# Kernel tuning notes

Hardware: AMD Instinct MI355X
Metric: run time of the kernel (lower is better)

Reference implementation:

```python
import jax, jax.numpy as jnp
import numpy as np

EPS = 1e-08
F_DIM = 512


def setup_inputs() -> dict:
    key = jax.random.key(0)
    ks = jax.random.split(key, 7)
    N, F = 50000, F_DIM
    q = jax.random.normal(ks[0], (N, 1, F), dtype=jnp.float32)
    mu = jax.random.normal(ks[1], (N, 3, F), dtype=jnp.float32)
    # Xavier-ish scaled params
    W_mix = jax.random.normal(ks[2], (2 * F, F), dtype=jnp.float32) * (1.0 / np.sqrt(F))
    W1 = jax.random.normal(ks[3], (F, 2 * F), dtype=jnp.float32) * (1.0 / np.sqrt(2 * F))
    b1 = jnp.zeros((F,), dtype=jnp.float32)
    W2 = jax.random.normal(ks[4], (3 * F, F), dtype=jnp.float32) * (1.0 / np.sqrt(F))
    b2 = jnp.zeros((3 * F,), dtype=jnp.float32)
    return {"q": q, "mu": mu, "W_mix": W_mix, "W1": W1, "b1": b1, "W2": W2, "b2": b2}


def reference(q, mu, W_mix, W1, b1, W2, b2):
    F = q.shape[-1]
    # mu_channel_mix: [N,3,F] @ [F,2F] -> [N,3,2F]
    mu_mix = jnp.einsum('ndf,gf->ndg', mu, W_mix)
    mu_V, mu_W = mu_mix[..., :F], mu_mix[..., F:]
    # vector norm over Cartesian axis -> [N,1,F]
    mu_Vn = jnp.sqrt(jnp.sum(mu_V * mu_V, axis=-2, keepdims=True) + EPS)
    ctx = jnp.concatenate([q, mu_Vn], axis=-1)  # [N,1,2F]
    h = jax.nn.silu(jnp.einsum('nsf,gf->nsg', ctx, W1) + b1)  # [N,1,F]
    x = jnp.einsum('nsf,gf->nsg', h, W2) + b2  # [N,1,3F]
    dq_intra = x[..., :F]
    dmu_intra = x[..., F:2 * F] * mu_W  # broadcast [N,1,F]*[N,3,F]
    dqmu_intra = x[..., 2 * F:] * jnp.sum(mu_V * mu_W, axis=1, keepdims=True)
    q_out = q + dq_intra + dqmu_intra
    mu_out = mu + dmu_intra
    return (q_out, mu_out)
```

## Files before the change

### kernel.cpp

```cpp
#include <hip/hip_runtime.h>
#include <stdint.h>

#define NN 50000
#define QWORDS 25600000

typedef __attribute__((ext_vector_type(8))) short bf16x8;
typedef __attribute__((ext_vector_type(4))) float f32x4;

__device__ __forceinline__ uint32_t f2bf(float x){
  uint32_t u = __builtin_bit_cast(uint32_t, x);
  u += 0x7FFFu + ((u >> 16) & 1u);
  return u >> 16;
}
__device__ __forceinline__ float bf2f(uint32_t b){
  uint32_t u = b << 16;
  return __builtin_bit_cast(float, u);
}
__device__ __forceinline__ void gload16(const uint16_t* g, uint16_t* l){
  __builtin_amdgcn_global_load_lds(
      (const __attribute__((address_space(1))) uint32_t*)g,
      (__attribute__((address_space(3))) uint32_t*)l, 16, 0, 0);
}
__device__ __forceinline__ f32x4 mfma16(bf16x8 a, bf16x8 b, f32x4 c){
  return __builtin_amdgcn_mfma_f32_16x16x32_bf16(a, b, c, 0, 0, 0);
}

#define FENCE() asm volatile("" ::: "memory")

__global__ void k_convert(const float* __restrict__ wmix, const float* __restrict__ w1,
                          const float* __restrict__ w2, uint16_t* __restrict__ dst){
  int i = blockIdx.x * 256 + threadIdx.x;
  int e = i << 2;
  const float* s; int o;
  if (e < 524288)       { s = wmix; o = e; }
  else if (e < 1048576) { s = w1;   o = e - 524288; }
  else                  { s = w2;   o = e - 1048576; }
  f32x4 v = *(const f32x4*)(s + o);
  uint2 pk;
  pk.x = f2bf(v[0]) | (f2bf(v[1]) << 16);
  pk.y = f2bf(v[2]) | (f2bf(v[3]) << 16);
  *(uint2*)(dst + e) = pk;
}

__global__ __launch_bounds__(512, 4)
void k_gemm1(const float* __restrict__ mu, const uint16_t* __restrict__ wmixb,
             uint16_t* __restrict__ qh, float* __restrict__ muW){
  __shared__ uint16_t As[2][12288];
  __shared__ uint16_t Bs[2][8192];
  const int tid  = threadIdx.x;
  const int lane = tid & 63;
  const int w    = tid >> 6;
  const int wn   = w & 3;
  const int wf   = w >> 2;
  const int orig = blockIdx.x;
  const int j    = (orig & 7) * 782 + (orig >> 3);
  const int f0   = (j & 7) * 64;
  const int n0   = (j >> 3) * 64;
  const int lrow = tid >> 4;
  const int lcol = (tid & 15) * 4;

  f32x4 ar[6];
  auto A_LOAD = [&](int ks){
    const int k0 = ks * 64;
    #pragma unroll
    for (int p=0; p<6; ++p){
      int r = p*32 + lrow;
      int d = r >> 6, nrow = r & 63;
      int n = n0 + nrow;
      int g = (n < NN ? n : NN-1)*3 + d;
      ar[p] = *(const f32x4*)(mu + (size_t)g*512 + k0 + lcol);
    }
  };
  auto A_WRITE = [&](int buf){
    #pragma unroll
    for (int p=0; p<6; ++p){
      int r = p*32 + lrow;
      f32x4 v = ar[p];
      uint2 pk;
      pk.x = f2bf(v[0]) | (f2bf(v[1]) << 16);
      pk.y = f2bf(v[2]) | (f2bf(v[3]) << 16);
      *(uint2*)&As[buf][r*64 + (lcol ^ ((r&7)<<3))] = pk;
    }
  };
  auto B_ISSUE = [&](int ks, int buf){
    const int k0 = ks * 64;
    #pragma unroll
    for (int jj=0; jj<2; ++jj){
      int jb = w*2 + jj;
      int row = jb*8 + (lane>>3);
      int g = (row < 64) ? (f0 + row) : (448 + f0 + row);
      int srcc = ((lane&7) ^ ((lane>>3)&7)) * 8;
      gload16(wmixb + (size_t)g*512 + k0 + srcc, &Bs[buf][jb*512]);
    }
  };

  const f32x4 z4 = {0.f,0.f,0.f,0.f};
  f32x4 acc[3][4];
  #pragma unroll
  for (int d=0; d<3; ++d)
    #pragma unroll
    for (int nt=0; nt<4; ++nt) acc[d][nt] = z4;

  A_LOAD(0); B_ISSUE(0, 0); A_WRITE(0);
  for (int ks=0; ks<8; ++ks){
    const int cur = ks & 1;
    __syncthreads();
    if (ks < 7){ A_LOAD(ks+1); B_ISSUE(ks+1, cur^1); }
    #pragma unroll
    for (int kf=0; kf<2; ++kf){
      int kc = kf*32 + (lane>>4)*8;
      bf16x8 af[3];
      #pragma unroll
      for (int d=0; d<3; ++d){
        int r = d*64 + wn*16 + (lane&15);
        af[d] = *(const bf16x8*)&As[cur][r*64 + (kc ^ ((r&7)<<3))];
      }
      #pragma unroll
      for (int nt=0; nt<4; ++nt){
        int ntg = wf*2 + (nt&1) + (nt>>1)*4;
        int rr = ntg*16 + (lane&15);
        bf16x8 bf = *(const bf16x8*)&Bs[cur][rr*64 + (kc ^ ((rr&7)<<3))];
        #pragma unroll
        for (int d=0; d<3; ++d)
          acc[d][nt] = mfma16(bf, af[d], acc[d][nt]);
      }
    }
    if (ks < 7) A_WRITE(cur^1);
  }

  const int rb4 = (lane >> 4) * 4;
  const int nthr = n0 + wn*16 + (lane & 15);
  if (nthr < NN){
    #pragma unroll
    for (int c=0; c<2; ++c){
      int f = f0 + (wf*2 + c)*16 + rb4;
      uint2 pkv, pkd; f32x4 u0v, u1v, u2v;
      uint32_t vb[4], db[4];
      #pragma unroll
      for (int p=0; p<4; ++p){
        float v0 = acc[0][c][p],   v1 = acc[1][c][p],   v2 = acc[2][c][p];
        float u0 = acc[0][c+2][p], u1 = acc[1][c+2][p], u2 = acc[2][c+2][p];
        float vn = sqrtf(v0*v0 + v1*v1 + v2*v2 + 1e-8f);
        float dt = v0*u0 + v1*u1 + v2*u2;
        vb[p] = f2bf(vn); db[p] = f2bf(dt);
        u0v[p] = u0; u1v[p] = u1; u2v[p] = u2;
      }
      pkv.x = vb[0] | (vb[1] << 16); pkv.y = vb[2] | (vb[3] << 16);
      pkd.x = db[0] | (db[1] << 16); pkd.y = db[2] | (db[3] << 16);
      *(uint2*)(qh + (size_t)nthr*1024 + f)       = pkv;
      *(uint2*)(qh + (size_t)nthr*1024 + 512 + f) = pkd;
      size_t mb = (size_t)nthr*1536 + f;
      *(f32x4*)(muW + mb)        = u0v;
      *(f32x4*)(muW + mb + 512)  = u1v;
      *(f32x4*)(muW + mb + 1024) = u2v;
    }
  }
}

__global__ __launch_bounds__(512, 4)
void k_gemm1b(const float* __restrict__ mu, const uint16_t* __restrict__ wmixb,
              uint16_t* __restrict__ qh, uint16_t* __restrict__ mw16){
  __shared__ uint16_t As[2][12288];
  __shared__ uint16_t Bs[2][8192];
  const int tid  = threadIdx.x;
  const int lane = tid & 63;
  const int w    = tid >> 6;
  const int wn   = w & 3;
  const int wf   = w >> 2;
  const int orig = blockIdx.x;
  const int j    = (orig & 7) * 782 + (orig >> 3);
  const int f0   = (j & 7) * 64;
  const int n0   = (j >> 3) * 64;
  const int lrow = tid >> 4;
  const int lcol = (tid & 15) * 4;

  f32x4 ar[6];
  auto A_LOAD = [&](int ks){
    const int k0 = ks * 64;
    #pragma unroll
    for (int p=0; p<6; ++p){
      int r = p*32 + lrow;
      int d = r >> 6, nrow = r & 63;
      int n = n0 + nrow;
      int g = (n < NN ? n : NN-1)*3 + d;
      ar[p] = *(const f32x4*)(mu + (size_t)g*512 + k0 + lcol);
    }
  };
  auto A_WRITE = [&](int buf){
    #pragma unroll
    for (int p=0; p<6; ++p){
      int r = p*32 + lrow;
      f32x4 v = ar[p];
      uint2 pk;
      pk.x = f2bf(v[0]) | (f2bf(v[1]) << 16);
      pk.y = f2bf(v[2]) | (f2bf(v[3]) << 16);
      *(uint2*)&As[buf][r*64 + (lcol ^ ((r&7)<<3))] = pk;
    }
  };
  auto B_ISSUE = [&](int ks, int buf){
    const int k0 = ks * 64;
    #pragma unroll
    for (int jj=0; jj<2; ++jj){
      int jb = w*2 + jj;
      int row = jb*8 + (lane>>3);
      int g = (row < 64) ? (f0 + row) : (448 + f0 + row);
      int srcc = ((lane&7) ^ ((lane>>3)&7)) * 8;
      gload16(wmixb + (size_t)g*512 + k0 + srcc, &Bs[buf][jb*512]);
    }
  };

  const f32x4 z4 = {0.f,0.f,0.f,0.f};
  f32x4 acc[3][4];
  #pragma unroll
  for (int d=0; d<3; ++d)
    #pragma unroll
    for (int nt=0; nt<4; ++nt) acc[d][nt] = z4;

  A_LOAD(0); B_ISSUE(0, 0); A_WRITE(0);
  for (int ks=0; ks<8; ++ks){
    const int cur = ks & 1;
    __syncthreads();
    if (ks < 7){ A_LOAD(ks+1); B_ISSUE(ks+1, cur^1); }
    #pragma unroll
    for (int kf=0; kf<2; ++kf){
      int kc = kf*32 + (lane>>4)*8;
      bf16x8 af[3];
      #pragma unroll
      for (int d=0; d<3; ++d){
        int r = d*64 + wn*16 + (lane&15);
        af[d] = *(const bf16x8*)&As[cur][r*64 + (kc ^ ((r&7)<<3))];
      }
      #pragma unroll
      for (int nt=0; nt<4; ++nt){
        int ntg = wf*2 + (nt&1) + (nt>>1)*4;
        int rr = ntg*16 + (lane&15);
        bf16x8 bf = *(const bf16x8*)&Bs[cur][rr*64 + (kc ^ ((rr&7)<<3))];
        #pragma unroll
        for (int d=0; d<3; ++d)
          acc[d][nt] = mfma16(bf, af[d], acc[d][nt]);
      }
    }
    if (ks < 7) A_WRITE(cur^1);
  }

  const int rb4 = (lane >> 4) * 4;
  const int nthr = n0 + wn*16 + (lane & 15);
  if (nthr < NN){
    #pragma unroll
    for (int c=0; c<2; ++c){
      int f = f0 + (wf*2 + c)*16 + rb4;
      uint2 pkv, pkd, pw0, pw1, pw2;
      uint32_t vb[4], db[4], w0[4], w1[4], w2[4];
      #pragma unroll
      for (int p=0; p<4; ++p){
        float v0 = acc[0][c][p],   v1 = acc[1][c][p],   v2 = acc[2][c][p];
        float u0 = acc[0][c+2][p], u1 = acc[1][c+2][p], u2 = acc[2][c+2][p];
        float vn = sqrtf(v0*v0 + v1*v1 + v2*v2 + 1e-8f);
        float dt = v0*u0 + v1*u1 + v2*u2;
        vb[p] = f2bf(vn); db[p] = f2bf(dt);
        w0[p] = f2bf(u0); w1[p] = f2bf(u1); w2[p] = f2bf(u2);
      }
      pkv.x = vb[0] | (vb[1] << 16); pkv.y = vb[2] | (vb[3] << 16);
      pkd.x = db[0] | (db[1] << 16); pkd.y = db[2] | (db[3] << 16);
      pw0.x = w0[0] | (w0[1] << 16); pw0.y = w0[2] | (w0[3] << 16);
      pw1.x = w1[0] | (w1[1] << 16); pw1.y = w1[2] | (w1[3] << 16);
      pw2.x = w2[0] | (w2[1] << 16); pw2.y = w2[2] | (w2[3] << 16);
      *(uint2*)(qh + (size_t)nthr*1024 + f)       = pkv;
      *(uint2*)(qh + (size_t)nthr*1024 + 512 + f) = pkd;
      size_t mb = (size_t)nthr*1536 + f;
      *(uint2*)(mw16 + mb)        = pw0;
      *(uint2*)(mw16 + mb + 512)  = pw1;
      *(uint2*)(mw16 + mb + 1024) = pw2;
    }
  }
}

__global__ __launch_bounds__(512, 4)
void k_gemm2(const float* __restrict__ q, const uint16_t* __restrict__ w1b,
             const float* __restrict__ b1, uint16_t* __restrict__ qh){
  __shared__ uint16_t A2[2][2048];
  __shared__ uint16_t B2[2][16384];
  const int tid  = threadIdx.x;
  const int lane = tid & 63;
  const int w    = tid >> 6;
  const int wm   = w >> 2;
  const int wn   = w & 3;
  const int n0   = blockIdx.x * 64;

  f32x4 qa;
  auto QA_LOAD = [&](int s){
    int k0 = s*32;
    int row = tid >> 3, ch = tid & 7;
    int nc = (n0 + row < NN) ? n0 + row : NN-1;
    qa = *(const f32x4*)(q + (size_t)nc*512 + k0 + ch*4);
  };
  auto QA_WRITE = [&](int buf){
    int row = tid >> 3, ch = tid & 7;
    uint2 pk;
    pk.x = f2bf(qa[0]) | (f2bf(qa[1]) << 16);
    pk.y = f2bf(qa[2]) | (f2bf(qa[3]) << 16);
    *(uint2*)&A2[buf][row*32 + (((ch>>1) ^ (row&3))<<3) + (ch&1)*4] = pk;
  };
  auto VA_ISSUE = [&](int s, int buf){
    if (w < 4){
      int k0v = (s-16)*32;
      int row = w*16 + (lane>>2);
      int nc = (n0 + row < NN) ? n0 + row : NN-1;
      int srcch = (lane&3) ^ (row&3);
      gload16(qh + (size_t)nc*1024 + k0v + srcch*8, &A2[buf][w*512]);
    }
  };
  auto B_ISSUE = [&](int s, int buf){
    int k0 = s*32;
    #pragma unroll
    for (int jj=0; jj<4; ++jj){
      int j = w*4 + jj;
      int row = j*16 + (lane>>2);
      int srcch = (lane&3) ^ (row&3);
      gload16(w1b + (size_t)row*1024 + k0 + srcch*8, &B2[buf][j*512]);
    }
  };

  const f32x4 z4 = {0.f,0.f,0.f,0.f};
  f32x4 acc2[2][8];
  #pragma unroll
  for (int mt=0; mt<2; ++mt)
    #pragma unroll
    for (int nt=0; nt<8; ++nt) acc2[mt][nt] = z4;

  QA_LOAD(0); B_ISSUE(0, 0); QA_WRITE(0);
  for (int s=0; s<32; ++s){
    const int cur = s & 1;
    __syncthreads();
    if (s < 31){
      if (s+1 < 16) QA_LOAD(s+1); else VA_ISSUE(s+1, cur^1);
      B_ISSUE(s+1, cur^1);
    }
    {
      int kc = (lane>>4)*8;
      bf16x8 a[2];
      #pragma unroll
      for (int mt=0; mt<2; ++mt){
        int r = wm*32 + mt*16 + (lane&15);
        a[mt] = *(const bf16x8*)&A2[cur][r*32 + (kc ^ ((r&3)<<3))];
      }
      #pragma unroll
      for (int nt=0; nt<8; ++nt){
        int rr = wn*128 + nt*16 + (lane&15);
        bf16x8 b = *(const bf16x8*)&B2[cur][rr*32 + (kc ^ ((rr&3)<<3))];
        acc2[0][nt] = mfma16(a[0], b, acc2[0][nt]);
        acc2[1][nt] = mfma16(a[1], b, acc2[1][nt]);
      }
    }
    if (s < 31 && s+1 < 16) QA_WRITE(cur^1);
  }

  const int rb4 = (lane >> 4) * 4;
  #pragma unroll
  for (int nt=0; nt<8; ++nt){
    int col = wn*128 + nt*16 + (lane&15);
    float bb = b1[col];
    #pragma unroll
    for (int mt=0; mt<2; ++mt)
      #pragma unroll
      for (int j=0; j<4; ++j){
        int n = n0 + wm*32 + mt*16 + rb4 + j;
        if (n < NN){
          float x = acc2[mt][nt][j] + bb;
          float sv = x / (1.f + __expf(-x));
          qh[(size_t)n*1024 + col] = (uint16_t)f2bf(sv);
        }
      }
  }
}

__global__ __launch_bounds__(256, 4)
void k_gemm3c(const float* __restrict__ q, const float* __restrict__ mu,
              const uint16_t* __restrict__ w2b, const float* __restrict__ b2,
              float* __restrict__ dout, const uint16_t* __restrict__ mw16){
  __shared__ uint16_t Hs[16*512];
  __shared__ uint16_t B3[2][6144];
  const int tid  = threadIdx.x;
  const int lane = tid & 63;
  const int w    = tid >> 6;
  const int n0   = blockIdx.x * 16;
  const uint16_t* qh = (const uint16_t*)dout;
  float* mout = dout + (size_t)QWORDS;
  const int l15 = lane & 15;
  const int rb4 = (lane >> 4) * 4;
  const f32x4 z4 = {0.f,0.f,0.f,0.f};

  #pragma unroll
  for (int i=0; i<4; ++i){
    int row = w*4 + i;
    int nc2 = (n0 + row < NN) ? n0 + row : NN-1;
    gload16(qh + (size_t)nc2*1024 + (size_t)((lane ^ (row&7))*8), &Hs[row*512]);
  }

  auto B_ISSUE = [&](int it, int ks, uint16_t* slot){
    #pragma unroll
    for (int jj=0; jj<3; ++jj){
      int j = w*3 + jj;
      int rr = j*16 + (lane>>2);
      int s3 = rr >> 6, fi = rr & 63;
      int g = s3*512 + it*64 + fi;
      int srcc = ((lane&3) ^ (rr&3)) * 8;
      gload16(w2b + (size_t)g*512 + ks*32 + srcc, slot + j*512);
    }
  };
  B_ISSUE(0, 0, B3[0]);

  const int nthr = n0 + l15;
  const int nc   = nthr < NN ? nthr : NN-1;

  f32x4 qv, bbv[3], muv[3], mwv[3];
  float dtv[4];
  int   fb = 0;
  f32x4 acc3[3];

#define K3C_MFMA(P) do{ \
    const uint16_t* bsl = B3[(P)&1]; \
    __builtin_amdgcn_s_setprio(1); \
    { \
      int r = l15; \
      int ch = ((P)*4 + (lane>>4)) ^ (r&7); \
      bf16x8 a = *(const bf16x8*)&Hs[r*512 + ch*8]; \
      _Pragma("unroll") \
      for (int s3=0; s3<3; ++s3){ \
        int rr = s3*64 + w*16 + l15; \
        int chb = (lane>>4) ^ (rr&3); \
        bf16x8 b = *(const bf16x8*)&bsl[rr*32 + chb*8]; \
        acc3[s3] = mfma16(b, a, acc3[s3]); \
      } \
    } \
    __builtin_amdgcn_s_setprio(0); \
  } while(0)

#define K3C_PHASE(P, WAIT) \
    asm volatile("s_waitcnt vmcnt(" #WAIT ")" ::: "memory"); \
    __builtin_amdgcn_s_barrier(); \
    B_ISSUE(it, (P)+1, B3[((P)+1)&1]); \
    FENCE(); \
    K3C_MFMA(P);

  #pragma unroll 1
  for (int it=0; it<8; ++it){
    if (it) { asm volatile("s_waitcnt vmcnt(4)" ::: "memory"); }
    else    { asm volatile("s_waitcnt vmcnt(0)" ::: "memory"); }
    __builtin_amdgcn_s_barrier();
    B_ISSUE(it, 1, B3[1]);
    FENCE();
    {
      #pragma unroll
      for (int s3=0; s3<3; ++s3) acc3[s3] = z4;
      fb = it*64 + w*16 + rb4;
      bbv[0] = *(const f32x4*)(b2 + fb);
      bbv[1] = *(const f32x4*)(b2 + 512 + fb);
      bbv[2] = *(const f32x4*)(b2 + 1024 + fb);
      uint2 du = *(const uint2*)(qh + (size_t)nc*1024 + 512 + fb);
      dtv[0] = bf2f(du.x & 0xffff); dtv[1] = bf2f(du.x >> 16);
      dtv[2] = bf2f(du.y & 0xffff); dtv[3] = bf2f(du.y >> 16);
      qv = *(const f32x4*)(q + (size_t)nc*512 + fb);
    }
    FENCE();
    K3C_MFMA(0);

    asm volatile("s_waitcnt vmcnt(5)" ::: "memory");
    __builtin_amdgcn_s_barrier();
    B_ISSUE(it, 2, B3[0]);
    FENCE();
    {
      size_t mb = (size_t)nc*1536 + fb;
      muv[0] = *(const f32x4*)(mu + mb);
      muv[1] = *(const f32x4*)(mu + mb + 512);
      muv[2] = *(const f32x4*)(mu + mb + 1024);
    }
    FENCE();
    K3C_MFMA(1);

    asm volatile("s_waitcnt vmcnt(3)" ::: "memory");
    __builtin_amdgcn_s_barrier();
    B_ISSUE(it, 3, B3[1]);
    FENCE();
    {
      size_t mb = (size_t)nc*1536 + fb;
      uint2 a0 = *(const uint2*)(mw16 + mb);
      uint2 a1 = *(const uint2*)(mw16 + mb + 512);
      uint2 a2 = *(const uint2*)(mw16 + mb + 1024);
      mwv[0][0]=bf2f(a0.x&0xffff); mwv[0][1]=bf2f(a0.x>>16);
      mwv[0][2]=bf2f(a0.y&0xffff); mwv[0][3]=bf2f(a0.y>>16);
      mwv[1][0]=bf2f(a1.x&0xffff); mwv[1][1]=bf2f(a1.x>>16);
      mwv[1][2]=bf2f(a1.y&0xffff); mwv[1][3]=bf2f(a1.y>>16);
      mwv[2][0]=bf2f(a2.x&0xffff); mwv[2][1]=bf2f(a2.x>>16);
      mwv[2][2]=bf2f(a2.y&0xffff); mwv[2][3]=bf2f(a2.y>>16);
    }
    FENCE();
    K3C_MFMA(2);

    K3C_PHASE(3, 3)
    K3C_PHASE(4, 0)
    K3C_PHASE(5, 0)
    K3C_PHASE(6, 0)
    K3C_PHASE(7, 0)
    K3C_PHASE(8, 0)
    K3C_PHASE(9, 0)
    K3C_PHASE(10, 0)
    K3C_PHASE(11, 0)
    K3C_PHASE(12, 0)
    K3C_PHASE(13, 0)
    K3C_PHASE(14, 0)

    asm volatile("s_waitcnt vmcnt(0)" ::: "memory");
    __builtin_amdgcn_s_barrier();
    if (it < 7) B_ISSUE(it+1, 0, B3[0]);
    FENCE();
    K3C_MFMA(15);
    if (nthr < NN){
      f32x4 qo, m0, m1, m2;
      #pragma unroll
      for (int p=0; p<4; ++p){
        float x0 = acc3[0][p] + bbv[0][p];
        float x1 = acc3[1][p] + bbv[1][p];
        float x2 = acc3[2][p] + bbv[2][p];
        qo[p] = qv[p] + x0 + x2*dtv[p];
        m0[p] = muv[0][p] + x1*mwv[0][p];
        m1[p] = muv[1][p] + x1*mwv[1][p];
        m2[p] = muv[2][p] + x1*mwv[2][p];
      }
      *(f32x4*)(dout + (size_t)nthr*512 + fb) = qo;
      size_t mb = (size_t)nthr*1536 + fb;
      *(f32x4*)(mout + mb)        = m0;
      *(f32x4*)(mout + mb + 512)  = m1;
      *(f32x4*)(mout + mb + 1024) = m2;
    }
  }
#undef K3C_PHASE
#undef K3C_MFMA
}

__global__ __launch_bounds__(512, 4)
void k_gemm3(const float* __restrict__ q, const float* __restrict__ mu,
             const uint16_t* __restrict__ w2b, const float* __restrict__ b2,
             float* __restrict__ dout){
  __shared__ uint16_t Hs[32*512];
  __shared__ uint16_t B3[2][12288];
  const int tid  = threadIdx.x;
  const int lane = tid & 63;
  const int w    = tid >> 6;
  const int wm   = w >> 2;
  const int wn   = w & 3;
  const int n0   = blockIdx.x * 32;
  const uint16_t* qh = (const uint16_t*)dout;
  float* mout = dout + (size_t)QWORDS;
  const int l15 = lane & 15;
  const int rb4 = (lane >> 4) * 4;
  const f32x4 z4 = {0.f,0.f,0.f,0.f};

  #pragma unroll
  for (int i=0; i<4; ++i){
    int row = w*4 + i;
    int nc2 = (n0 + row < NN) ? n0 + row : NN-1;
    gload16(qh + (size_t)nc2*1024 + (size_t)((lane ^ (row&7))*8), &Hs[row*512]);
  }

  auto B_ISSUE = [&](int it, int ks, uint16_t* slot){
    #pragma unroll
    for (int jj=0; jj<3; ++jj){
      int jx = w*3 + jj;
      int rr = jx*8 + (lane>>3);
      int s3 = rr >> 6, fi = rr & 63;
      int g = s3*512 + it*64 + fi;
      gload16(w2b + (size_t)g*512 + ks*64 + ((lane&7) ^ (rr&7))*8, slot + jx*512);
    }
  };
  B_ISSUE(0, 0, B3[0]);

  const int nthr = n0 + wm*16 + l15;
  const int nc   = nthr < NN ? nthr : NN-1;

  f32x4 qv, bbv[3], muv[3], mwv[3];
  float dtv[4];
  int   fb = 0;
  f32x4 acc3[3];

#define K3_MFMA(KS) do{ \
    const uint16_t* bsl = B3[(KS)&1]; \
    __builtin_amdgcn_s_setprio(1); \
    _Pragma("unroll") \
    for (int kf=0; kf<2; ++kf){ \
      int r = wm*16 + l15; \
      int ch = ((KS)*8 + kf*4 + (lane>>4)) ^ (r&7); \
      bf16x8 a = *(const bf16x8*)&Hs[r*512 + ch*8]; \
      _Pragma("unroll") \
      for (int s3=0; s3<3; ++s3){ \
        int rr = s3*64 + wn*16 + l15; \
        int chb = (kf*4 + (lane>>4)) ^ (rr&7); \
        bf16x8 b = *(const bf16x8*)&bsl[rr*64 + chb*8]; \
        acc3[s3] = mfma16(b, a, acc3[s3]); \
      } \
    } \
    __builtin_amdgcn_s_setprio(0); \
  } while(0)

  #pragma unroll 1
  for (int it=0; it<8; ++it){
    if (it) { asm volatile("s_waitcnt vmcnt(4)" ::: "memory"); }
    else    { asm volatile("s_waitcnt vmcnt(0)" ::: "memory"); }
    __builtin_amdgcn_s_barrier();
    B_ISSUE(it, 1, B3[1]);
    FENCE();
    {
      #pragma unroll
      for (int s3=0; s3<3; ++s3) acc3[s3] = z4;
      fb = it*64 + wn*16 + rb4;
      bbv[0] = *(const f32x4*)(b2 + fb);
      bbv[1] = *(const f32x4*)(b2 + 512 + fb);
      bbv[2] = *(const f32x4*)(b2 + 1024 + fb);
      uint2 du = *(const uint2*)(qh + (size_t)nc*1024 + 512 + fb);
      dtv[0] = bf2f(du.x & 0xffff); dtv[1] = bf2f(du.x >> 16);
      dtv[2] = bf2f(du.y & 0xffff); dtv[3] = bf2f(du.y >> 16);
      qv = *(const f32x4*)(q + (size_t)nc*512 + fb);
    }
    FENCE();
    K3_MFMA(0);

    asm volatile("s_waitcnt vmcnt(5)" ::: "memory");
    __builtin_amdgcn_s_barrier();
    B_ISSUE(it, 2, B3[0]);
    FENCE();
    {
      size_t mb = (size_t)nc*1536 + fb;
      muv[0] = *(const f32x4*)(mu + mb);
      muv[1] = *(const f32x4*)(mu + mb + 512);
      muv[2] = *(const f32x4*)(mu + mb + 1024);
    }
    FENCE();
    K3_MFMA(1);

    asm volatile("s_waitcnt vmcnt(3)" ::: "memory");
    __builtin_amdgcn_s_barrier();
    B_ISSUE(it, 3, B3[1]);
    FENCE();
    {
      size_t mb = (size_t)nc*1536 + fb;
      mwv[0] = *(const f32x4*)(mout + mb);
      mwv[1] = *(const f32x4*)(mout + mb + 512);
      mwv[2] = *(const f32x4*)(mout + mb + 1024);
    }
    FENCE();
    K3_MFMA(2);

    asm volatile("s_waitcnt vmcnt(3)" ::: "memory");
    __builtin_amdgcn_s_barrier();
    B_ISSUE(it, 4, B3[0]);
    FENCE();
    K3_MFMA(3);

    asm volatile("s_waitcnt vmcnt(0)" ::: "memory");
    __builtin_amdgcn_s_barrier();
    B_ISSUE(it, 5, B3[1]);
    FENCE();
    K3_MFMA(4);

    asm volatile("s_waitcnt vmcnt(0)" ::: "memory");
    __builtin_amdgcn_s_barrier();
    B_ISSUE(it, 6, B3[0]);
    FENCE();
    K3_MFMA(5);

    asm volatile("s_waitcnt vmcnt(0)" ::: "memory");
    __builtin_amdgcn_s_barrier();
    B_ISSUE(it, 7, B3[1]);
    FENCE();
    K3_MFMA(6);

    asm volatile("s_waitcnt vmcnt(0)" ::: "memory");
    __builtin_amdgcn_s_barrier();
    if (it < 7) B_ISSUE(it+1, 0, B3[0]);
    FENCE();
    K3_MFMA(7);
    if (nthr < NN){
      f32x4 qo, m0, m1, m2;
      #pragma unroll
      for (int p=0; p<4; ++p){
        float x0 = acc3[0][p] + bbv[0][p];
        float x1 = acc3[1][p] + bbv[1][p];
        float x2 = acc3[2][p] + bbv[2][p];
        qo[p] = qv[p] + x0 + x2*dtv[p];
        m0[p] = muv[0][p] + x1*mwv[0][p];
        m1[p] = muv[1][p] + x1*mwv[1][p];
        m2[p] = muv[2][p] + x1*mwv[2][p];
      }
      *(f32x4*)(dout + (size_t)nthr*512 + fb) = qo;
      size_t mb = (size_t)nthr*1536 + fb;
      *(f32x4*)(mout + mb)        = m0;
      *(f32x4*)(mout + mb + 512)  = m1;
      *(f32x4*)(mout + mb + 1024) = m2;
    }
  }
#undef K3_MFMA
}

extern "C" void kernel_launch(void* const* d_in, const int* in_sizes, int n_in,
                              void* d_out, int out_size, void* d_ws, size_t ws_size,
                              hipStream_t stream){
  (void)in_sizes; (void)n_in; (void)out_size;
  const float* q    = (const float*)d_in[0];
  const float* mu   = (const float*)d_in[1];
  const float* wmix = (const float*)d_in[2];
  const float* w1   = (const float*)d_in[3];
  const float* b1   = (const float*)d_in[4];
  const float* w2   = (const float*)d_in[5];
  const float* b2   = (const float*)d_in[6];
  uint16_t* wb = (uint16_t*)d_ws;
  float* dout = (float*)d_out;

  hipLaunchKernelGGL(k_convert, dim3(1792), dim3(256), 0, stream, wmix, w1, w2, wb);

  const size_t need = ((size_t)1835008 + (size_t)NN*1536) * 2;
  if (ws_size >= need){
    uint16_t* mw16 = wb + 1835008;
    hipLaunchKernelGGL(k_gemm1b, dim3(6256), dim3(512), 0, stream,
                       mu, wb, (uint16_t*)d_out, mw16);
    hipLaunchKernelGGL(k_gemm2, dim3(782), dim3(512), 0, stream,
                       q, wb + 524288, b1, (uint16_t*)d_out);
    hipLaunchKernelGGL(k_gemm3c, dim3(3125), dim3(256), 0, stream,
                       q, mu, wb + 1048576, b2, dout, mw16);
  } else {
    hipLaunchKernelGGL(k_gemm1, dim3(6256), dim3(512), 0, stream,
                       mu, wb, (uint16_t*)d_out, dout + (size_t)QWORDS);
    hipLaunchKernelGGL(k_gemm2, dim3(782), dim3(512), 0, stream,
                       q, wb + 524288, b1, (uint16_t*)d_out);
    hipLaunchKernelGGL(k_gemm3, dim3(1563), dim3(512), 0, stream,
                       q, mu, wb + 1048576, b2, dout);
  }
}
```

Measured before the change: 972.7 us.

## Warp-specialize final GEMM into producer and consumer waves with 32-row tiles

Replaces the 256-thread, 16-row third-GEMM kernel with a 512-thread kernel. Four waves only stream W2 tiles into a double-buffered LDS slot, and four compute waves each handle two 16-row MFMA groups over a wider K step of 64. Doubling the rows per block halves the weight traffic per output row. Moving global-to-LDS issue off the compute waves is meant to keep the MFMA stream uninterrupted. In exchange, half the waves do no math, the grid is halved and the block uses more LDS, which may lower occupancy and the overlap across blocks.

```diff
diff --git a/kernel.cpp b/kernel.cpp
--- a/kernel.cpp
+++ b/kernel.cpp
@@ -374,21 +374,20 @@
   }
 }
 
-__global__ __launch_bounds__(256, 4)
-void k_gemm3c(const float* __restrict__ q, const float* __restrict__ mu,
+__global__ __launch_bounds__(512, 4)
+void k_gemm3d(const float* __restrict__ q, const float* __restrict__ mu,
               const uint16_t* __restrict__ w2b, const float* __restrict__ b2,
               float* __restrict__ dout, const uint16_t* __restrict__ mw16){
-  __shared__ uint16_t Hs[16*512];
-  __shared__ uint16_t B3[2][6144];
+  __shared__ uint16_t Hs[32*512];
+  __shared__ uint16_t B3[2][12288];
   const int tid  = threadIdx.x;
   const int lane = tid & 63;
   const int w    = tid >> 6;
-  const int n0   = blockIdx.x * 16;
+  const int n0   = blockIdx.x * 32;
   const uint16_t* qh = (const uint16_t*)dout;
   float* mout = dout + (size_t)QWORDS;
   const int l15 = lane & 15;
   const int rb4 = (lane >> 4) * 4;
-  const f32x4 z4 = {0.f,0.f,0.f,0.f};
 
   #pragma unroll
   for (int i=0; i<4; ++i){
@@ -397,145 +396,163 @@
     gload16(qh + (size_t)nc2*1024 + (size_t)((lane ^ (row&7))*8), &Hs[row*512]);
   }
 
-  auto B_ISSUE = [&](int it, int ks, uint16_t* slot){
-    #pragma unroll
-    for (int jj=0; jj<3; ++jj){
-      int j = w*3 + jj;
-      int rr = j*16 + (lane>>2);
-      int s3 = rr >> 6, fi = rr & 63;
-      int g = s3*512 + it*64 + fi;
-      int srcc = ((lane&3) ^ (rr&3)) * 8;
-      gload16(w2b + (size_t)g*512 + ks*32 + srcc, slot + j*512);
-    }
-  };
-  B_ISSUE(0, 0, B3[0]);
-
-  const int nthr = n0 + l15;
-  const int nc   = nthr < NN ? nthr : NN-1;
-
-  f32x4 qv, bbv[3], muv[3], mwv[3];
-  float dtv[4];
-  int   fb = 0;
-  f32x4 acc3[3];
-
-#define K3C_MFMA(P) do{ \
-    const uint16_t* bsl = B3[(P)&1]; \
+  if (w >= 4){
+    const int pw = w - 4;
+    auto B_ISSUE = [&](int it, int ks){
+      uint16_t* slot = B3[ks & 1];
+      #pragma unroll
+      for (int jj=0; jj<6; ++jj){
+        int jx = pw*6 + jj;
+        int rr = jx*8 + (lane>>3);
+        int s3 = rr >> 6, fi = rr & 63;
+        int g = s3*512 + it*64 + fi;
+        gload16(w2b + (size_t)g*512 + ks*64 + ((lane&7) ^ (rr&7))*8, slot + jx*512);
+      }
+    };
+    B_ISSUE(0, 0);
+    asm volatile("s_waitcnt vmcnt(0)" ::: "memory");
+    __syncthreads();
+    #pragma unroll 1
+    for (int it=0; it<8; ++it){
+      #pragma unroll
+      for (int p=0; p<8; ++p){
+        int nit = it, nks = p+1;
+        if (nks == 8){ nks = 0; nit = it+1; }
+        if (nit < 8) B_ISSUE(nit, nks);
+        asm volatile("s_waitcnt vmcnt(0)" ::: "memory");
+        __builtin_amdgcn_s_barrier();
+      }
+    }
+  } else {
+    const int cw = w;
+    asm volatile("s_waitcnt vmcnt(0)" ::: "memory");
+    __syncthreads();
+    const int nth0 = n0 + l15, nth1 = n0 + 16 + l15;
+    const int nc0 = nth0 < NN ? nth0 : NN-1;
+    const int nc1 = nth1 < NN ? nth1 : NN-1;
+    const f32x4 z4 = {0.f,0.f,0.f,0.f};
+    f32x4 acc3[2][3];
+    f32x4 qv0, qv1, bbv[3], muv0[3], muv1[3];
+    uint2 du0, du1, mwu0[3], mwu1[3];
+    int fb = 0;
+
+#define K3D_MFMA(KS) do{ \
+    const uint16_t* bsl = B3[(KS)&1]; \
     __builtin_amdgcn_s_setprio(1); \
-    { \
-      int r = l15; \
-      int ch = ((P)*4 + (lane>>4)) ^ (r&7); \
-      bf16x8 a = *(const bf16x8*)&Hs[r*512 + ch*8]; \
+    _Pragma("unroll") \
+    for (int kf=0; kf<2; ++kf){ \
+      int ch = ((KS)*8 + kf*4 + (lane>>4)) ^ (l15&7); \
+      bf16x8 a0 = *(const bf16x8*)&Hs[l15*512 + ch*8]; \
+      bf16x8 a1 = *(const bf16x8*)&Hs[(16+l15)*512 + ch*8]; \
       _Pragma("unroll") \
       for (int s3=0; s3<3; ++s3){ \
-        int rr = s3*64 + w*16 + l15; \
-        int chb = (lane>>4) ^ (rr&3); \
-        bf16x8 b = *(const bf16x8*)&bsl[rr*32 + chb*8]; \
-        acc3[s3] = mfma16(b, a, acc3[s3]); \
+        int rr = s3*64 + cw*16 + l15; \
+        int chb = (kf*4 + (lane>>4)) ^ (rr&7); \
+        bf16x8 b = *(const bf16x8*)&bsl[rr*64 + chb*8]; \
+        acc3[0][s3] = mfma16(b, a0, acc3[0][s3]); \
+        acc3[1][s3] = mfma16(b, a1, acc3[1][s3]); \
       } \
     } \
     __builtin_amdgcn_s_setprio(0); \
   } while(0)
 
-#define K3C_PHASE(P, WAIT) \
-    asm volatile("s_waitcnt vmcnt(" #WAIT ")" ::: "memory"); \
-    __builtin_amdgcn_s_barrier(); \
-    B_ISSUE(it, (P)+1, B3[((P)+1)&1]); \
-    FENCE(); \
-    K3C_MFMA(P);
-
-  #pragma unroll 1
-  for (int it=0; it<8; ++it){
-    if (it) { asm volatile("s_waitcnt vmcnt(4)" ::: "memory"); }
-    else    { asm volatile("s_waitcnt vmcnt(0)" ::: "memory"); }
-    __builtin_amdgcn_s_barrier();
-    B_ISSUE(it, 1, B3[1]);
-    FENCE();
-    {
-      #pragma unroll
-      for (int s3=0; s3<3; ++s3) acc3[s3] = z4;
-      fb = it*64 + w*16 + rb4;
+    #pragma unroll 1
+    for (int it=0; it<8; ++it){
+      #pragma unroll
+      for (int m=0; m<2; ++m)
+        #pragma unroll
+        for (int s3=0; s3<3; ++s3) acc3[m][s3] = z4;
+      fb = it*64 + cw*16 + rb4;
       bbv[0] = *(const f32x4*)(b2 + fb);
       bbv[1] = *(const f32x4*)(b2 + 512 + fb);
       bbv[2] = *(const f32x4*)(b2 + 1024 + fb);
-      uint2 du = *(const uint2*)(qh + (size_t)nc*1024 + 512 + fb);
-      dtv[0] = bf2f(du.x & 0xffff); dtv[1] = bf2f(du.x >> 16);
-      dtv[2] = bf2f(du.y & 0xffff); dtv[3] = bf2f(du.y >> 16);
-      qv = *(const f32x4*)(q + (size_t)nc*512 + fb);
-    }
-    FENCE();
-    K3C_MFMA(0);
-
-    asm volatile("s_waitcnt vmcnt(5)" ::: "memory");
-    __builtin_amdgcn_s_barrier();
-    B_ISSUE(it, 2, B3[0]);
-    FENCE();
-    {
-      size_t mb = (size_t)nc*1536 + fb;
-      muv[0] = *(const f32x4*)(mu + mb);
-      muv[1] = *(const f32x4*)(mu + mb + 512);
-      muv[2] = *(const f32x4*)(mu + mb + 1024);
-    }
-    FENCE();
-    K3C_MFMA(1);
-
-    asm volatile("s_waitcnt vmcnt(3)" ::: "memory");
-    __builtin_amdgcn_s_barrier();
-    B_ISSUE(it, 3, B3[1]);
-    FENCE();
-    {
-      size_t mb = (size_t)nc*1536 + fb;
-      uint2 a0 = *(const uint2*)(mw16 + mb);
-      uint2 a1 = *(const uint2*)(mw16 + mb + 512);
-      uint2 a2 = *(const uint2*)(mw16 + mb + 1024);
-      mwv[0][0]=bf2f(a0.x&0xffff); mwv[0][1]=bf2f(a0.x>>16);
-      mwv[0][2]=bf2f(a0.y&0xffff); mwv[0][3]=bf2f(a0.y>>16);
-      mwv[1][0]=bf2f(a1.x&0xffff); mwv[1][1]=bf2f(a1.x>>16);
-      mwv[1][2]=bf2f(a1.y&0xffff); mwv[1][3]=bf2f(a1.y>>16);
-      mwv[2][0]=bf2f(a2.x&0xffff); mwv[2][1]=bf2f(a2.x>>16);
-      mwv[2][2]=bf2f(a2.y&0xffff); mwv[2][3]=bf2f(a2.y>>16);
-    }
-    FENCE();
-    K3C_MFMA(2);
-
-    K3C_PHASE(3, 3)
-    K3C_PHASE(4, 0)
-    K3C_PHASE(5, 0)
-    K3C_PHASE(6, 0)
-    K3C_PHASE(7, 0)
-    K3C_PHASE(8, 0)
-    K3C_PHASE(9, 0)
-    K3C_PHASE(10, 0)
-    K3C_PHASE(11, 0)
-    K3C_PHASE(12, 0)
-    K3C_PHASE(13, 0)
-    K3C_PHASE(14, 0)
-
-    asm volatile("s_waitcnt vmcnt(0)" ::: "memory");
-    __builtin_amdgcn_s_barrier();
-    if (it < 7) B_ISSUE(it+1, 0, B3[0]);
-    FENCE();
-    K3C_MFMA(15);
-    if (nthr < NN){
-      f32x4 qo, m0, m1, m2;
-      #pragma unroll
-      for (int p=0; p<4; ++p){
-        float x0 = acc3[0][p] + bbv[0][p];
-        float x1 = acc3[1][p] + bbv[1][p];
-        float x2 = acc3[2][p] + bbv[2][p];
-        qo[p] = qv[p] + x0 + x2*dtv[p];
-        m0[p] = muv[0][p] + x1*mwv[0][p];
-        m1[p] = muv[1][p] + x1*mwv[1][p];
-        m2[p] = muv[2][p] + x1*mwv[2][p];
-      }
-      *(f32x4*)(dout + (size_t)nthr*512 + fb) = qo;
-      size_t mb = (size_t)nthr*1536 + fb;
-      *(f32x4*)(mout + mb)        = m0;
-      *(f32x4*)(mout + mb + 512)  = m1;
-      *(f32x4*)(mout + mb + 1024) = m2;
-    }
-  }
-#undef K3C_PHASE
-#undef K3C_MFMA
+      du0 = *(const uint2*)(qh + (size_t)nc0*1024 + 512 + fb);
+      du1 = *(const uint2*)(qh + (size_t)nc1*1024 + 512 + fb);
+      qv0 = *(const f32x4*)(q + (size_t)nc0*512 + fb);
+      qv1 = *(const f32x4*)(q + (size_t)nc1*512 + fb);
+      FENCE();
+      K3D_MFMA(0);
+      __builtin_amdgcn_s_barrier();
+
+      {
+        size_t mb0 = (size_t)nc0*1536 + fb, mb1 = (size_t)nc1*1536 + fb;
+        muv0[0] = *(const f32x4*)(mu + mb0);
+        muv0[1] = *(const f32x4*)(mu + mb0 + 512);
+        muv0[2] = *(const f32x4*)(mu + mb0 + 1024);
+        muv1[0] = *(const f32x4*)(mu + mb1);
+        muv1[1] = *(const f32x4*)(mu + mb1 + 512);
+        muv1[2] = *(const f32x4*)(mu + mb1 + 1024);
+      }
+      FENCE();
+      K3D_MFMA(1);
+      __builtin_amdgcn_s_barrier();
+
+      {
+        size_t mb0 = (size_t)nc0*1536 + fb, mb1 = (size_t)nc1*1536 + fb;
+        mwu0[0] = *(const uint2*)(mw16 + mb0);
+        mwu0[1] = *(const uint2*)(mw16 + mb0 + 512);
+        mwu0[2] = *(const uint2*)(mw16 + mb0 + 1024);
+        mwu1[0] = *(const uint2*)(mw16 + mb1);
+        mwu1[1] = *(const uint2*)(mw16 + mb1 + 512);
+        mwu1[2] = *(const uint2*)(mw16 + mb1 + 1024);
+      }
+      FENCE();
+      K3D_MFMA(2);
+      __builtin_amdgcn_s_barrier();
+
+      K3D_MFMA(3); __builtin_amdgcn_s_barrier();
+      K3D_MFMA(4); __builtin_amdgcn_s_barrier();
+      K3D_MFMA(5); __builtin_amdgcn_s_barrier();
+      K3D_MFMA(6); __builtin_amdgcn_s_barrier();
+
+      K3D_MFMA(7);
+      asm volatile("s_waitcnt vmcnt(0)" ::: "memory");
+      {
+        auto dec = [&](uint2 u, int p)->float{
+          uint32_t h = (p & 2) ? u.y : u.x;
+          return bf2f((p & 1) ? (h >> 16) : (h & 0xffffu));
+        };
+        if (nth0 < NN){
+          f32x4 qo, mo0, mo1, mo2;
+          #pragma unroll
+          for (int p=0; p<4; ++p){
+            float x0 = acc3[0][0][p] + bbv[0][p];
+            float x1 = acc3[0][1][p] + bbv[1][p];
+            float x2 = acc3[0][2][p] + bbv[2][p];
+            qo[p]  = qv0[p] + x0 + x2*dec(du0, p);
+            mo0[p] = muv0[0][p] + x1*dec(mwu0[0], p);
+            mo1[p] = muv0[1][p] + x1*dec(mwu0[1], p);
+            mo2[p] = muv0[2][p] + x1*dec(mwu0[2], p);
+          }
+          *(f32x4*)(dout + (size_t)nth0*512 + fb) = qo;
+          size_t mb = (size_t)nth0*1536 + fb;
+          *(f32x4*)(mout + mb)        = mo0;
+          *(f32x4*)(mout + mb + 512)  = mo1;
+          *(f32x4*)(mout + mb + 1024) = mo2;
+        }
+        if (nth1 < NN){
+          f32x4 qo, mo0, mo1, mo2;
+          #pragma unroll
+          for (int p=0; p<4; ++p){
+            float x0 = acc3[1][0][p] + bbv[0][p];
+            float x1 = acc3[1][1][p] + bbv[1][p];
+            float x2 = acc3[1][2][p] + bbv[2][p];
+            qo[p]  = qv1[p] + x0 + x2*dec(du1, p);
+            mo0[p] = muv1[0][p] + x1*dec(mwu1[0], p);
+            mo1[p] = muv1[1][p] + x1*dec(mwu1[1], p);
+            mo2[p] = muv1[2][p] + x1*dec(mwu1[2], p);
+          }
+          *(f32x4*)(dout + (size_t)nth1*512 + fb) = qo;
+          size_t mb = (size_t)nth1*1536 + fb;
+          *(f32x4*)(mout + mb)        = mo0;
+          *(f32x4*)(mout + mb + 512)  = mo1;
+          *(f32x4*)(mout + mb + 1024) = mo2;
+        }
+      }
+      __builtin_amdgcn_s_barrier();
+    }
+#undef K3D_MFMA
+  }
 }
 
 __global__ __launch_bounds__(512, 4)
@@ -724,7 +741,7 @@
                        mu, wb, (uint16_t*)d_out, mw16);
     hipLaunchKernelGGL(k_gemm2, dim3(782), dim3(512), 0, stream,
                        q, wb + 524288, b1, (uint16_t*)d_out);
-    hipLaunchKernelGGL(k_gemm3c, dim3(3125), dim3(256), 0, stream,
+    hipLaunchKernelGGL(k_gemm3d, dim3(1563), dim3(512), 0, stream,
                        q, mu, wb + 1048576, b2, dout, mw16);
   } else {
     hipLaunchKernelGGL(k_gemm1, dim3(6256), dim3(512), 0, stream,
```

Result: faster. 899.6 us (-7.5%).

## Replace 16-row gemm3c with 32-row 512-thread gemm3b issuing epilogue loads early

Applied to the files above, without the earlier changes.

Swaps the final GEMM kernel from 16-row, 256-thread blocks with 16 k-phases to 32-row, 512-thread blocks with 8 k-phases of k=64. All epilogue operands (q, mu, the bf16 mu_W, the dt term) are loaded at the start of each output tile instead of spread across phases. The bf16 values are kept packed in registers and unpacked only in the epilogue to save registers. The aim is fewer barriers per tile and more reuse of each weight tile across rows, at the cost of larger blocks, more LDS per block, and long-latency loads held in flight.

```diff
diff --git a/kernel.cpp b/kernel.cpp
--- a/kernel.cpp
+++ b/kernel.cpp
@@ -374,174 +374,10 @@
   }
 }
 
-__global__ __launch_bounds__(256, 4)
-void k_gemm3c(const float* __restrict__ q, const float* __restrict__ mu,
+__global__ __launch_bounds__(512, 4)
+void k_gemm3b(const float* __restrict__ q, const float* __restrict__ mu,
               const uint16_t* __restrict__ w2b, const float* __restrict__ b2,
               float* __restrict__ dout, const uint16_t* __restrict__ mw16){
-  __shared__ uint16_t Hs[16*512];
-  __shared__ uint16_t B3[2][6144];
-  const int tid  = threadIdx.x;
-  const int lane = tid & 63;
-  const int w    = tid >> 6;
-  const int n0   = blockIdx.x * 16;
-  const uint16_t* qh = (const uint16_t*)dout;
-  float* mout = dout + (size_t)QWORDS;
-  const int l15 = lane & 15;
-  const int rb4 = (lane >> 4) * 4;
-  const f32x4 z4 = {0.f,0.f,0.f,0.f};
-
-  #pragma unroll
-  for (int i=0; i<4; ++i){
-    int row = w*4 + i;
-    int nc2 = (n0 + row < NN) ? n0 + row : NN-1;
-    gload16(qh + (size_t)nc2*1024 + (size_t)((lane ^ (row&7))*8), &Hs[row*512]);
-  }
-
-  auto B_ISSUE = [&](int it, int ks, uint16_t* slot){
-    #pragma unroll
-    for (int jj=0; jj<3; ++jj){
-      int j = w*3 + jj;
-      int rr = j*16 + (lane>>2);
-      int s3 = rr >> 6, fi = rr & 63;
-      int g = s3*512 + it*64 + fi;
-      int srcc = ((lane&3) ^ (rr&3)) * 8;
-      gload16(w2b + (size_t)g*512 + ks*32 + srcc, slot + j*512);
-    }
-  };
-  B_ISSUE(0, 0, B3[0]);
-
-  const int nthr = n0 + l15;
-  const int nc   = nthr < NN ? nthr : NN-1;
-
-  f32x4 qv, bbv[3], muv[3], mwv[3];
-  float dtv[4];
-  int   fb = 0;
-  f32x4 acc3[3];
-
-#define K3C_MFMA(P) do{ \
-    const uint16_t* bsl = B3[(P)&1]; \
-    __builtin_amdgcn_s_setprio(1); \
-    { \
-      int r = l15; \
-      int ch = ((P)*4 + (lane>>4)) ^ (r&7); \
-      bf16x8 a = *(const bf16x8*)&Hs[r*512 + ch*8]; \
-      _Pragma("unroll") \
-      for (int s3=0; s3<3; ++s3){ \
-        int rr = s3*64 + w*16 + l15; \
-        int chb = (lane>>4) ^ (rr&3); \
-        bf16x8 b = *(const bf16x8*)&bsl[rr*32 + chb*8]; \
-        acc3[s3] = mfma16(b, a, acc3[s3]); \
-      } \
-    } \
-    __builtin_amdgcn_s_setprio(0); \
-  } while(0)
-
-#define K3C_PHASE(P, WAIT) \
-    asm volatile("s_waitcnt vmcnt(" #WAIT ")" ::: "memory"); \
-    __builtin_amdgcn_s_barrier(); \
-    B_ISSUE(it, (P)+1, B3[((P)+1)&1]); \
-    FENCE(); \
-    K3C_MFMA(P);
-
-  #pragma unroll 1
-  for (int it=0; it<8; ++it){
-    if (it) { asm volatile("s_waitcnt vmcnt(4)" ::: "memory"); }
-    else    { asm volatile("s_waitcnt vmcnt(0)" ::: "memory"); }
-    __builtin_amdgcn_s_barrier();
-    B_ISSUE(it, 1, B3[1]);
-    FENCE();
-    {
-      #pragma unroll
-      for (int s3=0; s3<3; ++s3) acc3[s3] = z4;
-      fb = it*64 + w*16 + rb4;
-      bbv[0] = *(const f32x4*)(b2 + fb);
-      bbv[1] = *(const f32x4*)(b2 + 512 + fb);
-      bbv[2] = *(const f32x4*)(b2 + 1024 + fb);
-      uint2 du = *(const uint2*)(qh + (size_t)nc*1024 + 512 + fb);
-      dtv[0] = bf2f(du.x & 0xffff); dtv[1] = bf2f(du.x >> 16);
-      dtv[2] = bf2f(du.y & 0xffff); dtv[3] = bf2f(du.y >> 16);
-      qv = *(const f32x4*)(q + (size_t)nc*512 + fb);
-    }
-    FENCE();
-    K3C_MFMA(0);
-
-    asm volatile("s_waitcnt vmcnt(5)" ::: "memory");
-    __builtin_amdgcn_s_barrier();
-    B_ISSUE(it, 2, B3[0]);
-    FENCE();
-    {
-      size_t mb = (size_t)nc*1536 + fb;
-      muv[0] = *(const f32x4*)(mu + mb);
-      muv[1] = *(const f32x4*)(mu + mb + 512);
-      muv[2] = *(const f32x4*)(mu + mb + 1024);
-    }
-    FENCE();
-    K3C_MFMA(1);
-
-    asm volatile("s_waitcnt vmcnt(3)" ::: "memory");
-    __builtin_amdgcn_s_barrier();
-    B_ISSUE(it, 3, B3[1]);
-    FENCE();
-    {
-      size_t mb = (size_t)nc*1536 + fb;
-      uint2 a0 = *(const uint2*)(mw16 + mb);
-      uint2 a1 = *(const uint2*)(mw16 + mb + 512);
-      uint2 a2 = *(const uint2*)(mw16 + mb + 1024);
-      mwv[0][0]=bf2f(a0.x&0xffff); mwv[0][1]=bf2f(a0.x>>16);
-      mwv[0][2]=bf2f(a0.y&0xffff); mwv[0][3]=bf2f(a0.y>>16);
-      mwv[1][0]=bf2f(a1.x&0xffff); mwv[1][1]=bf2f(a1.x>>16);
-      mwv[1][2]=bf2f(a1.y&0xffff); mwv[1][3]=bf2f(a1.y>>16);
-      mwv[2][0]=bf2f(a2.x&0xffff); mwv[2][1]=bf2f(a2.x>>16);
-      mwv[2][2]=bf2f(a2.y&0xffff); mwv[2][3]=bf2f(a2.y>>16);
-    }
-    FENCE();
-    K3C_MFMA(2);
-
-    K3C_PHASE(3, 3)
-    K3C_PHASE(4, 0)
-    K3C_PHASE(5, 0)
-    K3C_PHASE(6, 0)
-    K3C_PHASE(7, 0)
-    K3C_PHASE(8, 0)
-    K3C_PHASE(9, 0)
-    K3C_PHASE(10, 0)
-    K3C_PHASE(11, 0)
-    K3C_PHASE(12, 0)
-    K3C_PHASE(13, 0)
-    K3C_PHASE(14, 0)
-
-    asm volatile("s_waitcnt vmcnt(0)" ::: "memory");
-    __builtin_amdgcn_s_barrier();
-    if (it < 7) B_ISSUE(it+1, 0, B3[0]);
-    FENCE();
-    K3C_MFMA(15);
-    if (nthr < NN){
-      f32x4 qo, m0, m1, m2;
-      #pragma unroll
-      for (int p=0; p<4; ++p){
-        float x0 = acc3[0][p] + bbv[0][p];
-        float x1 = acc3[1][p] + bbv[1][p];
-        float x2 = acc3[2][p] + bbv[2][p];
-        qo[p] = qv[p] + x0 + x2*dtv[p];
-        m0[p] = muv[0][p] + x1*mwv[0][p];
-        m1[p] = muv[1][p] + x1*mwv[1][p];
-        m2[p] = muv[2][p] + x1*mwv[2][p];
-      }
-      *(f32x4*)(dout + (size_t)nthr*512 + fb) = qo;
-      size_t mb = (size_t)nthr*1536 + fb;
-      *(f32x4*)(mout + mb)        = m0;
-      *(f32x4*)(mout + mb + 512)  = m1;
-      *(f32x4*)(mout + mb + 1024) = m2;
-    }
-  }
-#undef K3C_PHASE
-#undef K3C_MFMA
-}
-
-__global__ __launch_bounds__(512, 4)
-void k_gemm3(const float* __restrict__ q, const float* __restrict__ mu,
-             const uint16_t* __restrict__ w2b, const float* __restrict__ b2,
-             float* __restrict__ dout){
   __shared__ uint16_t Hs[32*512];
   __shared__ uint16_t B3[2][12288];
   const int tid  = threadIdx.x;
@@ -578,10 +414,10 @@
   const int nthr = n0 + wm*16 + l15;
   const int nc   = nthr < NN ? nthr : NN-1;
 
-  f32x4 qv, bbv[3], muv[3], mwv[3];
-  float dtv[4];
-  int   fb = 0;
-  f32x4 acc3[3];
+  f32x4 qv, bbv[3], muv[3];
+  uint2  du, mwu[3];
+  int    fb = 0;
+  f32x4  acc3[3];
 
 #define K3_MFMA(KS) do{ \
     const uint16_t* bsl = B3[(KS)&1]; \
@@ -616,6 +452,168 @@
       bbv[0] = *(const f32x4*)(b2 + fb);
       bbv[1] = *(const f32x4*)(b2 + 512 + fb);
       bbv[2] = *(const f32x4*)(b2 + 1024 + fb);
+      du = *(const uint2*)(qh + (size_t)nc*1024 + 512 + fb);
+      qv = *(const f32x4*)(q + (size_t)nc*512 + fb);
+      size_t mb = (size_t)nc*1536 + fb;
+      muv[0] = *(const f32x4*)(mu + mb);
+      muv[1] = *(const f32x4*)(mu + mb + 512);
+      muv[2] = *(const f32x4*)(mu + mb + 1024);
+      mwu[0] = *(const uint2*)(mw16 + mb);
+      mwu[1] = *(const uint2*)(mw16 + mb + 512);
+      mwu[2] = *(const uint2*)(mw16 + mb + 1024);
+    }
+    FENCE();
+    K3_MFMA(0);
+
+    asm volatile("s_waitcnt vmcnt(11)" ::: "memory");
+    __builtin_amdgcn_s_barrier();
+    B_ISSUE(it, 2, B3[0]);
+    FENCE();
+    K3_MFMA(1);
+
+    asm volatile("s_waitcnt vmcnt(0)" ::: "memory");
+    __builtin_amdgcn_s_barrier();
+    B_ISSUE(it, 3, B3[1]);
+    FENCE();
+    K3_MFMA(2);
+
+    asm volatile("s_waitcnt vmcnt(0)" ::: "memory");
+    __builtin_amdgcn_s_barrier();
+    B_ISSUE(it, 4, B3[0]);
+    FENCE();
+    K3_MFMA(3);
+
+    asm volatile("s_waitcnt vmcnt(0)" ::: "memory");
+    __builtin_amdgcn_s_barrier();
+    B_ISSUE(it, 5, B3[1]);
+    FENCE();
+    K3_MFMA(4);
+
+    asm volatile("s_waitcnt vmcnt(0)" ::: "memory");
+    __builtin_amdgcn_s_barrier();
+    B_ISSUE(it, 6, B3[0]);
+    FENCE();
+    K3_MFMA(5);
+
+    asm volatile("s_waitcnt vmcnt(0)" ::: "memory");
+    __builtin_amdgcn_s_barrier();
+    B_ISSUE(it, 7, B3[1]);
+    FENCE();
+    K3_MFMA(6);
+
+    asm volatile("s_waitcnt vmcnt(0)" ::: "memory");
+    __builtin_amdgcn_s_barrier();
+    if (it < 7) B_ISSUE(it+1, 0, B3[0]);
+    FENCE();
+    K3_MFMA(7);
+    if (nthr < NN){
+      f32x4 qo, m0, m1, m2;
+      #pragma unroll
+      for (int p=0; p<4; ++p){
+        uint32_t dh = (p & 2) ? du.y : du.x;
+        float dtp = bf2f((p & 1) ? (dh >> 16) : (dh & 0xffffu));
+        uint32_t w0h = (p & 2) ? mwu[0].y : mwu[0].x;
+        uint32_t w1h = (p & 2) ? mwu[1].y : mwu[1].x;
+        uint32_t w2h = (p & 2) ? mwu[2].y : mwu[2].x;
+        float mw0 = bf2f((p & 1) ? (w0h >> 16) : (w0h & 0xffffu));
+        float mw1 = bf2f((p & 1) ? (w1h >> 16) : (w1h & 0xffffu));
+        float mw2 = bf2f((p & 1) ? (w2h >> 16) : (w2h & 0xffffu));
+        float x0 = acc3[0][p] + bbv[0][p];
+        float x1 = acc3[1][p] + bbv[1][p];
+        float x2 = acc3[2][p] + bbv[2][p];
+        qo[p] = qv[p] + x0 + x2*dtp;
+        m0[p] = muv[0][p] + x1*mw0;
+        m1[p] = muv[1][p] + x1*mw1;
+        m2[p] = muv[2][p] + x1*mw2;
+      }
+      *(f32x4*)(dout + (size_t)nthr*512 + fb) = qo;
+      size_t mb = (size_t)nthr*1536 + fb;
+      *(f32x4*)(mout + mb)        = m0;
+      *(f32x4*)(mout + mb + 512)  = m1;
+      *(f32x4*)(mout + mb + 1024) = m2;
+    }
+  }
+#undef K3_MFMA
+}
+
+__global__ __launch_bounds__(512, 4)
+void k_gemm3(const float* __restrict__ q, const float* __restrict__ mu,
+             const uint16_t* __restrict__ w2b, const float* __restrict__ b2,
+             float* __restrict__ dout){
+  __shared__ uint16_t Hs[32*512];
+  __shared__ uint16_t B3[2][12288];
+  const int tid  = threadIdx.x;
+  const int lane = tid & 63;
+  const int w    = tid >> 6;
+  const int wm   = w >> 2;
+  const int wn   = w & 3;
+  const int n0   = blockIdx.x * 32;
+  const uint16_t* qh = (const uint16_t*)dout;
+  float* mout = dout + (size_t)QWORDS;
+  const int l15 = lane & 15;
+  const int rb4 = (lane >> 4) * 4;
+  const f32x4 z4 = {0.f,0.f,0.f,0.f};
+
+  #pragma unroll
+  for (int i=0; i<4; ++i){
+    int row = w*4 + i;
+    int nc2 = (n0 + row < NN) ? n0 + row : NN-1;
+    gload16(qh + (size_t)nc2*1024 + (size_t)((lane ^ (row&7))*8), &Hs[row*512]);
+  }
+
+  auto B_ISSUE = [&](int it, int ks, uint16_t* slot){
+    #pragma unroll
+    for (int jj=0; jj<3; ++jj){
+      int jx = w*3 + jj;
+      int rr = jx*8 + (lane>>3);
+      int s3 = rr >> 6, fi = rr & 63;
+      int g = s3*512 + it*64 + fi;
+      gload16(w2b + (size_t)g*512 + ks*64 + ((lane&7) ^ (rr&7))*8, slot + jx*512);
+    }
+  };
+  B_ISSUE(0, 0, B3[0]);
+
+  const int nthr = n0 + wm*16 + l15;
+  const int nc   = nthr < NN ? nthr : NN-1;
+
+  f32x4 qv, bbv[3], muv[3], mwv[3];
+  float dtv[4];
+  int   fb = 0;
+  f32x4 acc3[3];
+
+#define K3_MFMA(KS) do{ \
+    const uint16_t* bsl = B3[(KS)&1]; \
+    __builtin_amdgcn_s_setprio(1); \
+    _Pragma("unroll") \
+    for (int kf=0; kf<2; ++kf){ \
+      int r = wm*16 + l15; \
+      int ch = ((KS)*8 + kf*4 + (lane>>4)) ^ (r&7); \
+      bf16x8 a = *(const bf16x8*)&Hs[r*512 + ch*8]; \
+      _Pragma("unroll") \
+      for (int s3=0; s3<3; ++s3){ \
+        int rr = s3*64 + wn*16 + l15; \
+        int chb = (kf*4 + (lane>>4)) ^ (rr&7); \
+        bf16x8 b = *(const bf16x8*)&bsl[rr*64 + chb*8]; \
+        acc3[s3] = mfma16(b, a, acc3[s3]); \
+      } \
+    } \
+    __builtin_amdgcn_s_setprio(0); \
+  } while(0)
+
+  #pragma unroll 1
+  for (int it=0; it<8; ++it){
+    if (it) { asm volatile("s_waitcnt vmcnt(4)" ::: "memory"); }
+    else    { asm volatile("s_waitcnt vmcnt(0)" ::: "memory"); }
+    __builtin_amdgcn_s_barrier();
+    B_ISSUE(it, 1, B3[1]);
+    FENCE();
+    {
+      #pragma unroll
+      for (int s3=0; s3<3; ++s3) acc3[s3] = z4;
+      fb = it*64 + wn*16 + rb4;
+      bbv[0] = *(const f32x4*)(b2 + fb);
+      bbv[1] = *(const f32x4*)(b2 + 512 + fb);
+      bbv[2] = *(const f32x4*)(b2 + 1024 + fb);
       uint2 du = *(const uint2*)(qh + (size_t)nc*1024 + 512 + fb);
       dtv[0] = bf2f(du.x & 0xffff); dtv[1] = bf2f(du.x >> 16);
       dtv[2] = bf2f(du.y & 0xffff); dtv[3] = bf2f(du.y >> 16);
@@ -724,7 +722,7 @@
                        mu, wb, (uint16_t*)d_out, mw16);
     hipLaunchKernelGGL(k_gemm2, dim3(782), dim3(512), 0, stream,
                        q, wb + 524288, b1, (uint16_t*)d_out);
-    hipLaunchKernelGGL(k_gemm3c, dim3(3125), dim3(256), 0, stream,
+    hipLaunchKernelGGL(k_gemm3b, dim3(1563), dim3(512), 0, stream,
                        q, mu, wb + 1048576, b2, dout, mw16);
   } else {
     hipLaunchKernelGGL(k_gemm1, dim3(6256), dim3(512), 0, stream,
```

Measured after the change: 844.3 us, median of 2. 1.15x faster.
